# Kernel optimization log

Measured on AMD Instinct MI355X. Metric: run time of the kernel, lower is better.

## Reference

```python
import jax, jax.numpy as jnp
import numpy as np

DIM = 384; HEADS = 12; HD = DIM // HEADS; WS = 7; SHIFT = 3
RES = (14, 14, 14); N = WS ** 3; HID = 4 * DIM
NW = (RES[0] // WS) * (RES[1] // WS) * (RES[2] // WS)


def _np_attn_mask():
    Z, H, W = RES
    img = np.zeros((Z, H, W), np.float32)
    sl = (slice(0, -WS), slice(-WS, -SHIFT), slice(-SHIFT, None))
    cnt = 0
    for z in sl:
        for h in sl:
            for w in sl:
                img[z, h, w] = cnt
                cnt += 1
    m = img.reshape(Z // WS, WS, H // WS, WS, W // WS, WS)
    m = m.transpose(0, 2, 4, 1, 3, 5).reshape(NW, N)
    d = m[:, None, :] - m[:, :, None]
    return np.where(d != 0, -100.0, 0.0).astype(np.float32)  # [NW, N, N]


def _np_cpb_table_and_index():
    # continuous relative coords table, log-spaced (SwinV2), pretrained_window_size=0 -> normalize by WS-1
    r = np.arange(-(WS - 1), WS, dtype=np.float32)
    g = np.stack(np.meshgrid(r, r, r, indexing='ij'), -1)
    g = g / (WS - 1) * 8.0
    g = np.sign(g) * np.log2(np.abs(g) + 1.0) / np.log2(8.0)
    table = g.reshape(-1, 3)  # [(2W-1)^3, 3]
    c = np.stack(np.meshgrid(np.arange(WS), np.arange(WS), np.arange(WS), indexing='ij'))
    c = c.reshape(3, -1)  # [3, N]
    rel = c[:, :, None] - c[:, None, :] + (WS - 1)
    S = 2 * WS - 1
    idx = rel[0] * S * S + rel[1] * S + rel[2]  # [N, N]
    return table.astype(np.float32), idx.astype(np.int32)

_ATTN_MASK = _np_attn_mask()
_CPB_TABLE, _REL_IDX = _np_cpb_table_and_index()


def _ln(x, g, b, eps=1e-5):
    m = jnp.mean(x, -1, keepdims=True)
    v = jnp.mean(jnp.square(x - m), -1, keepdims=True)
    return (x - m) * jax.lax.rsqrt(v + eps) * g + b


def _win_part(x):  # [B,Z,H,W,C] -> [B*NW, WS,WS,WS, C]
    B, Z, H, W, C = x.shape
    x = x.reshape(B, Z // WS, WS, H // WS, WS, W // WS, WS, C)
    return x.transpose(0, 1, 3, 5, 2, 4, 6, 7).reshape(-1, WS, WS, WS, C)


def _win_rev(w, B):  # [B*NW, WS,WS,WS, C] -> [B,Z,H,W,C]
    Z, H, W = RES
    x = w.reshape(B, Z // WS, H // WS, W // WS, WS, WS, WS, -1)
    return x.transpose(0, 1, 4, 2, 5, 3, 6, 7).reshape(B, Z, H, W, -1)


def _forward(x, qkv_w, q_bias, v_bias, logit_scale, cpb_w1, cpb_b1, cpb_w2,
             proj_w, proj_b, norm1_g, norm1_b, norm2_g, norm2_b,
             fc1_w, fc1_b, fc2_w, fc2_b):
    Z, H, W = RES
    B, L, C = x.shape
    shortcut = x
    xg = x.reshape(B, Z, H, W, C)
    xg = jnp.roll(xg, (-SHIFT, -SHIFT, -SHIFT), axis=(1, 2, 3))
    xw = _win_part(xg).reshape(-1, N, C)  # [B*NW, N, C]

    qkv_b = jnp.concatenate([q_bias, jnp.zeros_like(q_bias), v_bias])
    qkv = xw @ qkv_w.T + qkv_b
    qkv = qkv.reshape(-1, N, 3, HEADS, HD).transpose(2, 0, 3, 1, 4)
    q, k, v = qkv[0], qkv[1], qkv[2]  # [B*NW, HEADS, N, HD]

    qn = q / jnp.maximum(jnp.linalg.norm(q, axis=-1, keepdims=True), 1e-12)
    kn = k / jnp.maximum(jnp.linalg.norm(k, axis=-1, keepdims=True), 1e-12)
    scale = jnp.exp(jnp.minimum(logit_scale, np.log(100.0)))  # [HEADS,1,1]
    attn = jnp.einsum('whnd,whmd->whnm', qn, kn) * scale

    # continuous relative position bias
    tbl = jax.nn.relu(jnp.asarray(_CPB_TABLE) @ cpb_w1.T + cpb_b1) @ cpb_w2.T  # [(2W-1)^3, HEADS]
    bias = 16.0 * jax.nn.sigmoid(tbl[_REL_IDX])  # [N, N, HEADS]
    attn = attn + bias.transpose(2, 0, 1)[None]

    mask = jnp.asarray(_ATTN_MASK)  # [NW, N, N]
    attn = attn.reshape(B, NW, HEADS, N, N) + mask[None, :, None]
    attn = jax.nn.softmax(attn.reshape(-1, HEADS, N, N), axis=-1)

    out = jnp.einsum('whnm,whmd->whnd', attn, v)
    out = out.transpose(0, 2, 1, 3).reshape(-1, N, C)
    out = out @ proj_w.T + proj_b

    xg = _win_rev(out.reshape(-1, WS, WS, WS, C), B)
    xg = jnp.roll(xg, (SHIFT, SHIFT, SHIFT), axis=(1, 2, 3))
    xa = xg.reshape(B, L, C)

    x1 = shortcut + _ln(xa, norm1_g, norm1_b)
    h = jax.nn.gelu(x1 @ fc1_w.T + fc1_b, approximate=False) @ fc2_w.T + fc2_b
    return x1 + _ln(h, norm2_g, norm2_b)


def setup_inputs() -> dict:
    key = jax.random.key(0)
    ks = jax.random.split(key, 8)
    B, L = 8, RES[0] * RES[1] * RES[2]
    s = 0.02
    return {
        'x': jax.random.normal(ks[0], (B, L, DIM), jnp.float32),
        'qkv_w': jax.random.normal(ks[1], (3 * DIM, DIM), jnp.float32) * s,
        'q_bias': jnp.zeros((DIM,), jnp.float32),
        'v_bias': jnp.zeros((DIM,), jnp.float32),
        'logit_scale': jnp.full((HEADS, 1, 1), np.log(10.0), jnp.float32),
        'cpb_w1': jax.random.normal(ks[2], (512, 3), jnp.float32) * s,
        'cpb_b1': jnp.zeros((512,), jnp.float32),
        'cpb_w2': jax.random.normal(ks[3], (HEADS, 512), jnp.float32) * s,
        'proj_w': jax.random.normal(ks[4], (DIM, DIM), jnp.float32) * s,
        'proj_b': jnp.zeros((DIM,), jnp.float32),
        'norm1_g': jnp.ones((DIM,), jnp.float32),
        'norm1_b': jnp.zeros((DIM,), jnp.float32),
        'norm2_g': jnp.ones((DIM,), jnp.float32),
        'norm2_b': jnp.zeros((DIM,), jnp.float32),
        'fc1_w': jax.random.normal(ks[5], (HID, DIM), jnp.float32) * s,
        'fc1_b': jnp.zeros((HID,), jnp.float32),
        'fc2_w': jax.random.normal(ks[6], (DIM, HID), jnp.float32) * s,
        'fc2_b': jnp.zeros((DIM,), jnp.float32),
    }


def reference(x, qkv_w, q_bias, v_bias, logit_scale, cpb_w1, cpb_b1, cpb_w2,
              proj_w, proj_b, norm1_g, norm1_b, norm2_g, norm2_b,
              fc1_w, fc1_b, fc2_w, fc2_b):
    return _forward(x, qkv_w, q_bias, v_bias, logit_scale, cpb_w1, cpb_b1, cpb_w2,
                    proj_w, proj_b, norm1_g, norm1_b, norm2_g, norm2_b,
                    fc1_w, fc1_b, fc2_w, fc2_b)
```

## Files before the change

### kernel.cpp

```cpp
#include <hip/hip_runtime.h>
#include <hip/hip_bf16.h>
#include <stdint.h>

namespace {

typedef __attribute__((ext_vector_type(8))) short s8v;
typedef __attribute__((ext_vector_type(4))) float f4v;
typedef __attribute__((ext_vector_type(8))) unsigned short us8;

constexpr int kN    = 343;
constexpr size_t kPlaneE = 768ull * 343 * 32;

__device__ __forceinline__ int regionOf(int c) { return c < 7 ? 0 : (c < 11 ? 1 : 2); }

__device__ __forceinline__ int winRowMap(int wtok) {
  int w = wtok / kN, nn = wtok % kN;
  int bb = w >> 3, nwi = w & 7;
  int nz = nn / 49, nh = (nn / 7) % 7, nw = nn % 7;
  int uz = (((nwi >> 2) & 1) * 7 + nz + 3) % 14;
  int uh = (((nwi >> 1) & 1) * 7 + nh + 3) % 14;
  int uw = (((nwi     ) & 1) * 7 + nw + 3) % 14;
  return bb * 2744 + uz * 196 + uh * 14 + uw;
}

__device__ __forceinline__ unsigned short f2bf(float f) {
  union { float f; unsigned u; } a; a.f = f;
  unsigned r = a.u + 0x7fffu + ((a.u >> 16) & 1u);
  return (unsigned short)(r >> 16);
}
__device__ __forceinline__ float bf2f(unsigned short u) {
  union { unsigned u; float f; } a; a.u = ((unsigned)u) << 16; return a.f;
}

__device__ __forceinline__ void gload16(const void* g, void* l) {
  __builtin_amdgcn_global_load_lds(
      (const __attribute__((address_space(1))) unsigned int*)g,
      (__attribute__((address_space(3))) unsigned int*)l, 16, 0, 0);
}

__device__ __forceinline__ float cpbFeat(int i) {
  float v = (float)(i - 6) * (8.0f / 6.0f);
  float a = log2f(fabsf(v) + 1.0f) * (1.0f / 3.0f);
  return v < 0.0f ? -a : a;
}

__global__ __launch_bounds__(256) void cvt_bf16_kernel(
    const float* __restrict__ src, unsigned short* __restrict__ dst, int n8) {
  int i = blockIdx.x * 256 + threadIdx.x;
  if (i >= n8) return;
  const float* s = src + (size_t)i * 8;
  float4 a = *(const float4*)s;
  float4 b = *(const float4*)(s + 4);
  us8 o;
  o[0]=f2bf(a.x); o[1]=f2bf(a.y); o[2]=f2bf(a.z); o[3]=f2bf(a.w);
  o[4]=f2bf(b.x); o[5]=f2bf(b.y); o[6]=f2bf(b.z); o[7]=f2bf(b.w);
  *(us8*)(dst + (size_t)i * 8) = o;
}

__global__ __launch_bounds__(256) void gather_x_kernel(
    const float* __restrict__ x, unsigned short* __restrict__ xg) {
  int chunk = blockIdx.x * 256 + threadIdx.x;
  if (chunk >= 21952 * 48) return;
  int wtok = chunk / 48, c = (chunk - wtok * 48) * 8;
  long row = winRowMap(wtok);
  const float* s = x + row * 384 + c;
  float4 a = *(const float4*)s;
  float4 b = *(const float4*)(s + 4);
  us8 o;
  o[0]=f2bf(a.x); o[1]=f2bf(a.y); o[2]=f2bf(a.z); o[3]=f2bf(a.w);
  o[4]=f2bf(b.x); o[5]=f2bf(b.y); o[6]=f2bf(b.z); o[7]=f2bf(b.w);
  *(us8*)(xg + (size_t)wtok * 384 + c) = o;
}

__global__ __launch_bounds__(256) void cpb_table_kernel(
    const float* __restrict__ w1, const float* __restrict__ b1,
    const float* __restrict__ w2, float* __restrict__ tbl) {
  int t = blockIdx.x * 256 + threadIdx.x;
  if (t >= 2197 * 12) return;
  int row = t / 12, h = t - (t / 12) * 12;
  float f0 = cpbFeat(row / 169), f1 = cpbFeat((row / 13) % 13), f2 = cpbFeat(row % 13);
  float acc = 0.f;
  for (int j = 0; j < 512; ++j) {
    float hid = fmaf(f0, w1[j*3+0], fmaf(f1, w1[j*3+1], fmaf(f2, w1[j*3+2], b1[j])));
    hid = fmaxf(hid, 0.f);
    acc = fmaf(hid, w2[h*512 + j], acc);
  }
  tbl[row * 12 + h] = acc;
}

__global__ __launch_bounds__(256) void cpb_bias_frag_kernel(
    const float* __restrict__ tbl, float* __restrict__ biasf) {
  int gid = blockIdx.x * 256 + threadIdx.x;
  if (gid >= 12 * 22 * 22 * 64) return;
  int lane = gid & 63, tile = gid >> 6;
  int jt = tile % 22, it = (tile / 22) % 22, h = tile / 484;
  int j = jt * 16 + (lane & 15);
  float v[4];
  #pragma unroll
  for (int r = 0; r < 4; ++r) {
    int i = it * 16 + (lane >> 4) * 4 + r;
    float val = -30000.f;
    if (i < kN && j < kN) {
      int iz = i/49, ih = (i/7)%7, iw = i%7;
      int jz = j/49, jh = (j/7)%7, jw = j%7;
      int idx = (iz-jz+6)*169 + (ih-jh+6)*13 + (iw-jw+6);
      float tv = tbl[idx*12 + h];
      val = 16.f / (1.f + __expf(-tv));
    }
    v[r] = val;
  }
  float4* dst = (float4*)(biasf + ((size_t)tile << 8) + (lane << 2));
  *dst = make_float4(v[0], v[1], v[2], v[3]);
}

template <int MODE>
__global__ __launch_bounds__(256) void gemm_bf16(
    const unsigned short* __restrict__ A, const unsigned short* __restrict__ W,
    const float* __restrict__ b0, const float* __restrict__ b1,
    void* __restrict__ outv, int K, int N) {
  __shared__ __align__(16) unsigned short As[2][64][32];
  __shared__ __align__(16) unsigned short Bs[2][128][32];
  const int tid = threadIdx.x, lane = tid & 63, wid = tid >> 6;
  const int wr = wid >> 1, wc = wid & 1;
  const int lr = lane & 15, lc = lane >> 4;
  const int m0 = blockIdx.y * 64, n0 = blockIdx.x * 128;

  const int sr = lane >> 2, sc = (lane & 3) << 3;
  const unsigned short* ga  = A + (size_t)(m0 + wid * 16 + sr) * K + sc;
  const unsigned short* gb0 = W + (size_t)(n0 + wid * 32 + sr) * K + sc;
  const unsigned short* gb1 = gb0 + (size_t)16 * K;

  f4v acc[2][4];
  const f4v zero4 = {0.f, 0.f, 0.f, 0.f};
  #pragma unroll
  for (int i = 0; i < 2; ++i)
    #pragma unroll
    for (int j = 0; j < 4; ++j) acc[i][j] = zero4;

  const int nk = K >> 5;
  gload16(ga,  &As[0][wid*16][0]);
  gload16(gb0, &Bs[0][wid*32][0]);
  gload16(gb1, &Bs[0][wid*32 + 16][0]);
  __syncthreads();
  for (int kt = 0; kt < nk; ++kt) {
    int cur = kt & 1;
    if (kt + 1 < nk) {
      gload16(ga  + (kt+1)*32, &As[cur^1][wid*16][0]);
      gload16(gb0 + (kt+1)*32, &Bs[cur^1][wid*32][0]);
      gload16(gb1 + (kt+1)*32, &Bs[cur^1][wid*32 + 16][0]);
    }
    s8v af0 = *(const s8v*)&As[cur][wr*32 + lr][lc*8];
    s8v af1 = *(const s8v*)&As[cur][wr*32 + 16 + lr][lc*8];
    #pragma unroll
    for (int ni = 0; ni < 4; ++ni) {
      s8v bf = *(const s8v*)&Bs[cur][wc*64 + ni*16 + lr][lc*8];
      acc[0][ni] = __builtin_amdgcn_mfma_f32_16x16x32_bf16(af0, bf, acc[0][ni], 0, 0, 0);
      acc[1][ni] = __builtin_amdgcn_mfma_f32_16x16x32_bf16(af1, bf, acc[1][ni], 0, 0, 0);
    }
    __syncthreads();
  }

  if (MODE == 0) {
    unsigned short* qkv = (unsigned short*)outv;
    #pragma unroll
    for (int mi = 0; mi < 2; ++mi)
      #pragma unroll
      for (int ni = 0; ni < 4; ++ni) {
        int cg = n0 + wc*64 + ni*16 + lr;
        int which = cg / 384, rem = cg - which * 384;
        const float* bp = (which == 0) ? b0 : (which == 2 ? b1 : nullptr);
        float badd = bp ? bp[rem] : 0.f;
        unsigned short* plane = qkv + (size_t)which * kPlaneE;
        #pragma unroll
        for (int r = 0; r < 4; ++r) {
          int mg = m0 + wr*32 + mi*16 + lc*4 + r;
          int w = mg / kN, nn = mg - w * kN;
          plane[((size_t)(w * 12 + (rem >> 5)) * kN + nn) * 32 + (rem & 31)] =
              f2bf(acc[mi][ni][r] + badd);
        }
      }
  } else {
    #pragma unroll
    for (int mi = 0; mi < 2; ++mi)
      #pragma unroll
      for (int ni = 0; ni < 4; ++ni) {
        int cg = n0 + wc*64 + ni*16 + lr;
        float badd = b0[cg];
        #pragma unroll
        for (int r = 0; r < 4; ++r) {
          size_t mg = (size_t)(m0 + wr*32 + mi*16 + lc*4 + r);
          float t = acc[mi][ni][r] + badd;
          if (MODE == 2) {
            t = 0.5f * t * (1.f + erff(t * 0.70710678118f));
            ((unsigned short*)outv)[mg * N + cg] = f2bf(t);
          } else {
            ((float*)outv)[mg * N + cg] = t;
          }
        }
      }
  }
}

__global__ __launch_bounds__(512) void attn_mfma(
    const unsigned short* __restrict__ qp, const unsigned short* __restrict__ kp,
    const unsigned short* __restrict__ vp, const float* __restrict__ biasf,
    const float* __restrict__ ls, unsigned short* __restrict__ outb) {
  __shared__ __align__(16) unsigned short Ksh[352][40];
  __shared__ __align__(16) unsigned short Vt[32][360];
  __shared__ __align__(16) unsigned short ps[8][16][360];
  __shared__ float qinvS[352], kinvS[352], cntS[352];

  const int wh = blockIdx.x;
  const int w = wh / 12, h = wh - w * 12;
  const int nwi = w & 7;
  const int tid = threadIdx.x, lane = tid & 63, wid = tid >> 6;
  const unsigned short* qb = qp + (size_t)wh * kN * 32;
  const unsigned short* kb = kp + (size_t)wh * kN * 32;
  const unsigned short* vb = vp + (size_t)wh * kN * 32;
  const float scale = __expf(fminf(ls[h], 4.6051702f));

  for (int idx = tid; idx < 1408; idx += 512) {
    int r = idx >> 2, c8 = (idx & 3) << 3;
    us8 v = {0,0,0,0,0,0,0,0};
    if (r < kN) v = *(const us8*)(kb + r * 32 + c8);
    *(us8*)&Ksh[r][c8] = v;
  }
  for (int idx = tid; idx < 32 * 17; idx += 512) {
    int d = idx / 17, c = kN + (idx - (idx / 17) * 17);
    Vt[d][c] = 0;
  }
  for (int idx = tid; idx < 1372; idx += 512) {
    int r = idx >> 2, c8 = (idx & 3) << 3;
    us8 v = *(const us8*)(vb + r * 32 + c8);
    #pragma unroll
    for (int e = 0; e < 8; ++e) Vt[c8 + e][r] = v[e];
  }
  for (int t = tid; t < 352; t += 512) {
    if (t < kN) {
      float qs = 0.f, ks = 0.f;
      #pragma unroll
      for (int c8 = 0; c8 < 4; ++c8) {
        us8 qv = *(const us8*)(qb + t * 32 + c8 * 8);
        us8 kv = *(const us8*)(kb + t * 32 + c8 * 8);
        #pragma unroll
        for (int e = 0; e < 8; ++e) {
          float f = bf2f(qv[e]); qs = fmaf(f, f, qs);
          float g = bf2f(kv[e]); ks = fmaf(g, g, ks);
        }
      }
      qinvS[t] = scale / fmaxf(sqrtf(qs), 1e-12f);
      kinvS[t] = 1.f / fmaxf(sqrtf(ks), 1e-12f);
      int jz = t / 49, jh = (t / 7) % 7, jw = t % 7;
      cntS[t] = (float)(regionOf(((nwi >> 2) & 1) * 7 + jz) * 9 +
                        regionOf(((nwi >> 1) & 1) * 7 + jh) * 3 +
                        regionOf(((nwi     ) & 1) * 7 + jw));
    } else {
      qinvS[t] = 1.f; kinvS[t] = 0.f; cntS[t] = 0.f;
    }
  }
  __syncthreads();

  const int lr = lane & 15, lc = lane >> 4;
  const f4v zero4 = {0.f, 0.f, 0.f, 0.f};

  for (int mt = wid; mt < 22; mt += 8) {
    const int i0 = mt * 16;
    s8v qa = *(const s8v*)(qb + (size_t)(i0 + lr) * 32 + lc * 8);
    float qi[4], ci[4];
    #pragma unroll
    for (int r = 0; r < 4; ++r) {
      qi[r] = qinvS[i0 + lc * 4 + r];
      ci[r] = cntS[i0 + lc * 4 + r];
    }
    float sreg[22][4];
    #pragma unroll
    for (int jt = 0; jt < 22; ++jt) {
      s8v kf = *(const s8v*)&Ksh[jt * 16 + lr][lc * 8];
      f4v s4 = __builtin_amdgcn_mfma_f32_16x16x32_bf16(qa, kf, zero4, 0, 0, 0);
      float kj = kinvS[jt * 16 + lr];
      float cj = cntS[jt * 16 + lr];
      float4 bq = *(const float4*)(biasf + (((size_t)(h * 22 + mt) * 22 + jt) << 8) + (lane << 2));
      sreg[jt][0] = s4[0] * qi[0] * kj + bq.x + ((cj != ci[0]) ? -100.f : 0.f);
      sreg[jt][1] = s4[1] * qi[1] * kj + bq.y + ((cj != ci[1]) ? -100.f : 0.f);
      sreg[jt][2] = s4[2] * qi[2] * kj + bq.z + ((cj != ci[2]) ? -100.f : 0.f);
      sreg[jt][3] = s4[3] * qi[3] * kj + bq.w + ((cj != ci[3]) ? -100.f : 0.f);
    }
    float mx[4] = {-3e38f, -3e38f, -3e38f, -3e38f};
    #pragma unroll
    for (int jt = 0; jt < 22; ++jt)
      #pragma unroll
      for (int r = 0; r < 4; ++r) mx[r] = fmaxf(mx[r], sreg[jt][r]);
    #pragma unroll
    for (int off = 1; off < 16; off <<= 1)
      #pragma unroll
      for (int r = 0; r < 4; ++r) mx[r] = fmaxf(mx[r], __shfl_xor(mx[r], off));
    float sum[4] = {0.f, 0.f, 0.f, 0.f};
    #pragma unroll
    for (int jt = 0; jt < 22; ++jt)
      #pragma unroll
      for (int r = 0; r < 4; ++r) {
        float p = __expf(sreg[jt][r] - mx[r]);
        sum[r] += p;
        ps[wid][lc * 4 + r][jt * 16 + lr] = f2bf(p);
      }
    #pragma unroll
    for (int off = 1; off < 16; off <<= 1)
      #pragma unroll
      for (int r = 0; r < 4; ++r) sum[r] += __shfl_xor(sum[r], off);
    float rinv[4];
    #pragma unroll
    for (int r = 0; r < 4; ++r) rinv[r] = 1.f / sum[r];

    f4v o0 = zero4, o1 = zero4;
    #pragma unroll
    for (int ks = 0; ks < 11; ++ks) {
      s8v pa = *(const s8v*)&ps[wid][lr][ks * 32 + lc * 8];
      s8v v0 = *(const s8v*)&Vt[lr][ks * 32 + lc * 8];
      s8v v1 = *(const s8v*)&Vt[16 + lr][ks * 32 + lc * 8];
      o0 = __builtin_amdgcn_mfma_f32_16x16x32_bf16(pa, v0, o0, 0, 0, 0);
      o1 = __builtin_amdgcn_mfma_f32_16x16x32_bf16(pa, v1, o1, 0, 0, 0);
    }
    #pragma unroll
    for (int r = 0; r < 4; ++r) {
      int i = i0 + lc * 4 + r;
      if (i < kN) {
        size_t base = ((size_t)(w * kN + i)) * 384 + h * 32;
        outb[base + lr]      = f2bf(o0[r] * rinv[r]);
        outb[base + 16 + lr] = f2bf(o1[r] * rinv[r]);
      }
    }
  }
}

template <int GATHER, int WBF>
__global__ __launch_bounds__(64) void ln_kernel(
    const float* __restrict__ src, const float* __restrict__ resid,
    const float* __restrict__ g, const float* __restrict__ b,
    float* __restrict__ out, unsigned short* __restrict__ outbf) {
  int row = blockIdx.x, lane = threadIdx.x;
  long dst = GATHER ? (long)winRowMap(row) : (long)row;
  float t[6];
  float sum = 0.f, sq = 0.f;
  #pragma unroll
  for (int i = 0; i < 6; ++i) {
    t[i] = src[(long)row * 384 + i * 64 + lane];
    sum += t[i];
    sq = fmaf(t[i], t[i], sq);
  }
  #pragma unroll
  for (int o = 32; o; o >>= 1) { sum += __shfl_xor(sum, o); sq += __shfl_xor(sq, o); }
  float mean = sum * (1.f / 384.f);
  float var = sq * (1.f / 384.f) - mean * mean;
  float rs = rsqrtf(var + 1e-5f);
  #pragma unroll
  for (int i = 0; i < 6; ++i) {
    int c = i * 64 + lane;
    float val = resid[dst * 384 + c] + (t[i] - mean) * rs * g[c] + b[c];
    out[dst * 384 + c] = val;
    if (WBF) outbf[dst * 384 + c] = f2bf(val);
  }
}

}

extern "C" void kernel_launch(void* const* d_in, const int* in_sizes, int n_in,
                              void* d_out, int out_size, void* d_ws, size_t ws_size,
                              hipStream_t stream) {
  const float* x      = (const float*)d_in[0];
  const float* qkv_w  = (const float*)d_in[1];
  const float* q_bias = (const float*)d_in[2];
  const float* v_bias = (const float*)d_in[3];
  const float* lscale = (const float*)d_in[4];
  const float* cpb_w1 = (const float*)d_in[5];
  const float* cpb_b1 = (const float*)d_in[6];
  const float* cpb_w2 = (const float*)d_in[7];
  const float* proj_w = (const float*)d_in[8];
  const float* proj_b = (const float*)d_in[9];
  const float* n1g    = (const float*)d_in[10];
  const float* n1b    = (const float*)d_in[11];
  const float* n2g    = (const float*)d_in[12];
  const float* n2b    = (const float*)d_in[13];
  const float* fc1_w  = (const float*)d_in[14];
  const float* fc1_b  = (const float*)d_in[15];
  const float* fc2_w  = (const float*)d_in[16];
  const float* fc2_b  = (const float*)d_in[17];
  float* outp = (float*)d_out;
  char* wsb = (char*)d_ws;

  float*          biasf = (float*)(wsb + 0);
  float*          tbl   = (float*)(wsb + 5947392);
  unsigned short* qkvp  = (unsigned short*)(wsb + 6052864);
  unsigned short* xg    = (unsigned short*)(wsb + 56630272);
  unsigned short* attno = (unsigned short*)(wsb + 73489408);
  unsigned short* wts   = (unsigned short*)(wsb + 90348544);
  float*          projt = (float*)(wsb + 93887488);
  float*          x1    = (float*)(wsb + 127605760);
  unsigned short* x1b   = (unsigned short*)(wsb + 161324032);
  unsigned short* hbuf  = qkvp;
  float*          h2    = projt;

  unsigned short* wq  = wts;
  unsigned short* wpj = wts + 442368;
  unsigned short* wf1 = wts + 589824;
  unsigned short* wf2 = wts + 1179648;

  cvt_bf16_kernel<<<216, 256, 0, stream>>>(qkv_w, wq, 55296);
  cvt_bf16_kernel<<<72,  256, 0, stream>>>(proj_w, wpj, 18432);
  cvt_bf16_kernel<<<288, 256, 0, stream>>>(fc1_w, wf1, 73728);
  cvt_bf16_kernel<<<288, 256, 0, stream>>>(fc2_w, wf2, 73728);
  gather_x_kernel<<<4116, 256, 0, stream>>>(x, xg);
  cpb_table_kernel<<<103, 256, 0, stream>>>(cpb_w1, cpb_b1, cpb_w2, tbl);
  cpb_bias_frag_kernel<<<1452, 256, 0, stream>>>(tbl, biasf);

  gemm_bf16<0><<<dim3(9, 343), 256, 0, stream>>>(xg, wq, q_bias, v_bias, qkvp, 384, 1152);

  attn_mfma<<<768, 512, 0, stream>>>(qkvp, qkvp + kPlaneE, qkvp + 2 * kPlaneE,
                                     biasf, lscale, attno);

  gemm_bf16<1><<<dim3(3, 343), 256, 0, stream>>>(attno, wpj, proj_b, nullptr, projt, 384, 384);

  ln_kernel<1, 1><<<21952, 64, 0, stream>>>(projt, x, n1g, n1b, x1, x1b);

  gemm_bf16<2><<<dim3(12, 343), 256, 0, stream>>>(x1b, wf1, fc1_b, nullptr, hbuf, 384, 1536);

  gemm_bf16<1><<<dim3(3, 343), 256, 0, stream>>>(hbuf, wf2, fc2_b, nullptr, h2, 1536, 384);

  ln_kernel<0, 0><<<21952, 64, 0, stream>>>(h2, x1, n2g, n2b, outp, nullptr);
}
```

Baseline: 360.8 us.

## Enlarge GEMM tiles, rework attention softmax in registers, pack LayerNorm rows

GEMM tiles grow from 64x128 to 128x128, so each block computes a 4x4 MFMA fragment grid and the grid shrinks to 172 row blocks, with padded rows guarded in the QKV epilogue. Attention now pre-normalises K in LDS and folds the Q norm, the logit scale and log2(e) into Q. It computes S transposed, so the softmax probabilities stay in registers as 16x16x16 MFMA operands instead of going through shared memory, and it uses exp2 and packed bf16 converts. LayerNorm packs 4 rows per 256-thread block, and the attention grid is reordered head-major. The padded GEMM rows read and write past the valid data, which is why the workspace offsets were enlarged.

Result: slower. 391.2 us (+8.4%).

```diff
diff --git a/kernel.cpp b/kernel.cpp
--- a/kernel.cpp
+++ b/kernel.cpp
@@ -5,11 +5,15 @@
 namespace {
 
 typedef __attribute__((ext_vector_type(8))) short s8v;
+typedef __attribute__((ext_vector_type(4))) short s4v;
 typedef __attribute__((ext_vector_type(4))) float f4v;
 typedef __attribute__((ext_vector_type(8))) unsigned short us8;
 
-constexpr int kN    = 343;
+constexpr int kN = 343;
 constexpr size_t kPlaneE = 768ull * 343 * 32;
+constexpr int kM = 21952;
+constexpr int kMp = 22016;
+constexpr float kL2E = 1.44269504f;
 
 __device__ __forceinline__ int regionOf(int c) { return c < 7 ? 0 : (c < 11 ? 1 : 2); }
 
@@ -31,6 +35,30 @@
 __device__ __forceinline__ float bf2f(unsigned short u) {
   union { unsigned u; float f; } a; a.u = ((unsigned)u) << 16; return a.f;
 }
+__device__ __forceinline__ unsigned cvtpk(float lo, float hi) {
+  unsigned r;
+  asm("v_cvt_pk_bf16_f32 %0, %1, %2" : "=v"(r) : "v"(lo), "v"(hi));
+  return r;
+}
+__device__ __forceinline__ float fexp2(float x) {
+#if __has_builtin(__builtin_amdgcn_exp2f)
+  return __builtin_amdgcn_exp2f(x);
+#else
+  return exp2f(x);
+#endif
+}
+
+#if __has_builtin(__builtin_amdgcn_mfma_f32_16x16x16bf16_1k)
+__device__ __forceinline__ f4v mfma16(s4v a, s4v b, f4v c) {
+  return __builtin_amdgcn_mfma_f32_16x16x16bf16_1k(a, b, c, 0, 0, 0);
+}
+#else
+__device__ __forceinline__ f4v mfma16(s4v a, s4v b, f4v c) {
+  f4v d;
+  asm("v_mfma_f32_16x16x16_bf16 %0, %1, %2, %3" : "=v"(d) : "v"(a), "v"(b), "v"(c));
+  return d;
+}
+#endif
 
 __device__ __forceinline__ void gload16(const void* g, void* l) {
   __builtin_amdgcn_global_load_lds(
@@ -60,7 +88,7 @@
 __global__ __launch_bounds__(256) void gather_x_kernel(
     const float* __restrict__ x, unsigned short* __restrict__ xg) {
   int chunk = blockIdx.x * 256 + threadIdx.x;
-  if (chunk >= 21952 * 48) return;
+  if (chunk >= kM * 48) return;
   int wtok = chunk / 48, c = (chunk - wtok * 48) * 8;
   long row = winRowMap(wtok);
   const float* s = x + row * 384 + c;
@@ -93,24 +121,24 @@
   int gid = blockIdx.x * 256 + threadIdx.x;
   if (gid >= 12 * 22 * 22 * 64) return;
   int lane = gid & 63, tile = gid >> 6;
-  int jt = tile % 22, it = (tile / 22) % 22, h = tile / 484;
-  int j = jt * 16 + (lane & 15);
+  int jt = tile % 22, qt = (tile / 22) % 22, h = tile / 484;
+  int i = qt * 16 + (lane & 15);
+  int j0 = jt * 16 + ((lane >> 4) << 2);
   float v[4];
   #pragma unroll
   for (int r = 0; r < 4; ++r) {
-    int i = it * 16 + (lane >> 4) * 4 + r;
-    float val = -30000.f;
+    int j = j0 + r;
+    float val = -43000.f;
     if (i < kN && j < kN) {
       int iz = i/49, ih = (i/7)%7, iw = i%7;
       int jz = j/49, jh = (j/7)%7, jw = j%7;
       int idx = (iz-jz+6)*169 + (ih-jh+6)*13 + (iw-jw+6);
       float tv = tbl[idx*12 + h];
-      val = 16.f / (1.f + __expf(-tv));
+      val = (16.f / (1.f + __expf(-tv))) * kL2E;
     }
     v[r] = val;
   }
-  float4* dst = (float4*)(biasf + ((size_t)tile << 8) + (lane << 2));
-  *dst = make_float4(v[0], v[1], v[2], v[3]);
+  *(float4*)(biasf + ((size_t)tile << 8) + (lane << 2)) = make_float4(v[0], v[1], v[2], v[3]);
 }
 
 template <int MODE>
@@ -118,78 +146,85 @@
     const unsigned short* __restrict__ A, const unsigned short* __restrict__ W,
     const float* __restrict__ b0, const float* __restrict__ b1,
     void* __restrict__ outv, int K, int N) {
-  __shared__ __align__(16) unsigned short As[2][64][32];
+  __shared__ __align__(16) unsigned short As[2][128][32];
   __shared__ __align__(16) unsigned short Bs[2][128][32];
   const int tid = threadIdx.x, lane = tid & 63, wid = tid >> 6;
   const int wr = wid >> 1, wc = wid & 1;
-  const int lr = lane & 15, lc = lane >> 4;
-  const int m0 = blockIdx.y * 64, n0 = blockIdx.x * 128;
-
-  const int sr = lane >> 2, sc = (lane & 3) << 3;
-  const unsigned short* ga  = A + (size_t)(m0 + wid * 16 + sr) * K + sc;
-  const unsigned short* gb0 = W + (size_t)(n0 + wid * 32 + sr) * K + sc;
-  const unsigned short* gb1 = gb0 + (size_t)16 * K;
-
-  f4v acc[2][4];
+  const int lq = lane & 15, gq = lane >> 4;
+  const int m0 = blockIdx.y * 128, n0 = blockIdx.x * 128;
+
+  const int r0 = tid >> 2, c0 = (tid & 3) << 3;
+  const unsigned short* gA0 = A + (size_t)(m0 + r0) * K + c0;
+  const unsigned short* gA1 = A + (size_t)(m0 + 64 + r0) * K + c0;
+  const unsigned short* gB0 = W + (size_t)(n0 + r0) * K + c0;
+  const unsigned short* gB1 = W + (size_t)(n0 + 64 + r0) * K + c0;
+
+  f4v acc[4][4];
   const f4v zero4 = {0.f, 0.f, 0.f, 0.f};
   #pragma unroll
-  for (int i = 0; i < 2; ++i)
+  for (int i = 0; i < 4; ++i)
     #pragma unroll
     for (int j = 0; j < 4; ++j) acc[i][j] = zero4;
 
   const int nk = K >> 5;
-  gload16(ga,  &As[0][wid*16][0]);
-  gload16(gb0, &Bs[0][wid*32][0]);
-  gload16(gb1, &Bs[0][wid*32 + 16][0]);
+#define STAGE(buf, kt)                                         \
+  gload16(gA0 + (kt) * 32, &As[buf][r0][c0]);                  \
+  gload16(gA1 + (kt) * 32, &As[buf][64 + r0][c0]);             \
+  gload16(gB0 + (kt) * 32, &Bs[buf][r0][c0]);                  \
+  gload16(gB1 + (kt) * 32, &Bs[buf][64 + r0][c0]);
+
+  STAGE(0, 0);
   __syncthreads();
   for (int kt = 0; kt < nk; ++kt) {
     int cur = kt & 1;
-    if (kt + 1 < nk) {
-      gload16(ga  + (kt+1)*32, &As[cur^1][wid*16][0]);
-      gload16(gb0 + (kt+1)*32, &Bs[cur^1][wid*32][0]);
-      gload16(gb1 + (kt+1)*32, &Bs[cur^1][wid*32 + 16][0]);
-    }
-    s8v af0 = *(const s8v*)&As[cur][wr*32 + lr][lc*8];
-    s8v af1 = *(const s8v*)&As[cur][wr*32 + 16 + lr][lc*8];
-    #pragma unroll
-    for (int ni = 0; ni < 4; ++ni) {
-      s8v bf = *(const s8v*)&Bs[cur][wc*64 + ni*16 + lr][lc*8];
-      acc[0][ni] = __builtin_amdgcn_mfma_f32_16x16x32_bf16(af0, bf, acc[0][ni], 0, 0, 0);
-      acc[1][ni] = __builtin_amdgcn_mfma_f32_16x16x32_bf16(af1, bf, acc[1][ni], 0, 0, 0);
+    if (kt + 1 < nk) { STAGE(cur ^ 1, kt + 1); }
+    s8v af[4];
+    #pragma unroll
+    for (int mt = 0; mt < 4; ++mt)
+      af[mt] = *(const s8v*)&As[cur][wr * 64 + mt * 16 + lq][gq * 8];
+    #pragma unroll
+    for (int nt = 0; nt < 4; ++nt) {
+      s8v bfr = *(const s8v*)&Bs[cur][wc * 64 + nt * 16 + lq][gq * 8];
+      #pragma unroll
+      for (int mt = 0; mt < 4; ++mt)
+        acc[mt][nt] = __builtin_amdgcn_mfma_f32_16x16x32_bf16(af[mt], bfr, acc[mt][nt], 0, 0, 0);
     }
     __syncthreads();
   }
+#undef STAGE
 
   if (MODE == 0) {
     unsigned short* qkv = (unsigned short*)outv;
     #pragma unroll
-    for (int mi = 0; mi < 2; ++mi)
-      #pragma unroll
-      for (int ni = 0; ni < 4; ++ni) {
-        int cg = n0 + wc*64 + ni*16 + lr;
-        int which = cg / 384, rem = cg - which * 384;
-        const float* bp = (which == 0) ? b0 : (which == 2 ? b1 : nullptr);
-        float badd = bp ? bp[rem] : 0.f;
-        unsigned short* plane = qkv + (size_t)which * kPlaneE;
+    for (int nt = 0; nt < 4; ++nt) {
+      int cg = n0 + wc * 64 + nt * 16 + lq;
+      int which = cg / 384, rem = cg - which * 384;
+      const float* bp = (which == 0) ? b0 : (which == 2 ? b1 : nullptr);
+      float badd = bp ? bp[rem] : 0.f;
+      unsigned short* plane = qkv + (size_t)which * kPlaneE;
+      #pragma unroll
+      for (int mt = 0; mt < 4; ++mt)
         #pragma unroll
         for (int r = 0; r < 4; ++r) {
-          int mg = m0 + wr*32 + mi*16 + lc*4 + r;
-          int w = mg / kN, nn = mg - w * kN;
-          plane[((size_t)(w * 12 + (rem >> 5)) * kN + nn) * 32 + (rem & 31)] =
-              f2bf(acc[mi][ni][r] + badd);
+          int mg = m0 + wr * 64 + mt * 16 + gq * 4 + r;
+          if (mg < kM) {
+            int w = mg / kN, nn = mg - w * kN;
+            plane[((size_t)(w * 12 + (rem >> 5)) * kN + nn) * 32 + (rem & 31)] =
+                f2bf(acc[mt][nt][r] + badd);
+          }
         }
-      }
+    }
   } else {
     #pragma unroll
-    for (int mi = 0; mi < 2; ++mi)
-      #pragma unroll
-      for (int ni = 0; ni < 4; ++ni) {
-        int cg = n0 + wc*64 + ni*16 + lr;
-        float badd = b0[cg];
+    for (int nt = 0; nt < 4; ++nt) {
+      int cg = n0 + wc * 64 + nt * 16 + lq;
+      float badd = b0[cg];
+      #pragma unroll
+      for (int mt = 0; mt < 4; ++mt)
         #pragma unroll
         for (int r = 0; r < 4; ++r) {
-          size_t mg = (size_t)(m0 + wr*32 + mi*16 + lc*4 + r);
-          float t = acc[mi][ni][r] + badd;
+          size_t mg = (size_t)(m0 + wr * 64 + mt * 16 + gq * 4 + r);
+          float t = acc[mt][nt][r] + badd;
           if (MODE == 2) {
             t = 0.5f * t * (1.f + erff(t * 0.70710678118f));
             ((unsigned short*)outv)[mg * N + cg] = f2bf(t);
@@ -197,7 +232,7 @@
             ((float*)outv)[mg * N + cg] = t;
           }
         }
-      }
+    }
   }
 }
 
@@ -206,138 +241,150 @@
     const unsigned short* __restrict__ vp, const float* __restrict__ biasf,
     const float* __restrict__ ls, unsigned short* __restrict__ outb) {
   __shared__ __align__(16) unsigned short Ksh[352][40];
-  __shared__ __align__(16) unsigned short Vt[32][360];
-  __shared__ __align__(16) unsigned short ps[8][16][360];
-  __shared__ float qinvS[352], kinvS[352], cntS[352];
-
-  const int wh = blockIdx.x;
-  const int w = wh / 12, h = wh - w * 12;
+  __shared__ __align__(16) unsigned short Vt[32][364];
+  __shared__ float qmulS[352];
+  __shared__ float cntS[352];
+
+  const int bid = blockIdx.x;
+  const int h = bid >> 6, w = bid & 63;
+  const int wh = w * 12 + h;
   const int nwi = w & 7;
   const int tid = threadIdx.x, lane = tid & 63, wid = tid >> 6;
+  const int lq = lane & 15, gq = lane >> 4;
   const unsigned short* qb = qp + (size_t)wh * kN * 32;
   const unsigned short* kb = kp + (size_t)wh * kN * 32;
   const unsigned short* vb = vp + (size_t)wh * kN * 32;
-  const float scale = __expf(fminf(ls[h], 4.6051702f));
+  const float sl2e = __expf(fminf(ls[h], 4.6051702f)) * kL2E;
 
   for (int idx = tid; idx < 1408; idx += 512) {
     int r = idx >> 2, c8 = (idx & 3) << 3;
-    us8 v = {0,0,0,0,0,0,0,0};
+    us8 v = {0, 0, 0, 0, 0, 0, 0, 0};
     if (r < kN) v = *(const us8*)(kb + r * 32 + c8);
     *(us8*)&Ksh[r][c8] = v;
   }
-  for (int idx = tid; idx < 32 * 17; idx += 512) {
-    int d = idx / 17, c = kN + (idx - (idx / 17) * 17);
-    Vt[d][c] = 0;
-  }
+  for (int idx = tid; idx < 288; idx += 512)
+    Vt[idx / 9][343 + (idx % 9)] = 0;
   for (int idx = tid; idx < 1372; idx += 512) {
     int r = idx >> 2, c8 = (idx & 3) << 3;
     us8 v = *(const us8*)(vb + r * 32 + c8);
     #pragma unroll
     for (int e = 0; e < 8; ++e) Vt[c8 + e][r] = v[e];
   }
-  for (int t = tid; t < 352; t += 512) {
+  __syncthreads();
+  if (tid < 352) {
+    int t = tid;
     if (t < kN) {
-      float qs = 0.f, ks = 0.f;
+      float ks = 0.f;
+      us8 kv[4];
       #pragma unroll
       for (int c8 = 0; c8 < 4; ++c8) {
-        us8 qv = *(const us8*)(qb + t * 32 + c8 * 8);
-        us8 kv = *(const us8*)(kb + t * 32 + c8 * 8);
+        kv[c8] = *(const us8*)&Ksh[t][c8 * 8];
         #pragma unroll
-        for (int e = 0; e < 8; ++e) {
-          float f = bf2f(qv[e]); qs = fmaf(f, f, qs);
-          float g = bf2f(kv[e]); ks = fmaf(g, g, ks);
-        }
+        for (int e = 0; e < 8; ++e) { float f = bf2f(kv[c8][e]); ks = fmaf(f, f, ks); }
       }
-      qinvS[t] = scale / fmaxf(sqrtf(qs), 1e-12f);
-      kinvS[t] = 1.f / fmaxf(sqrtf(ks), 1e-12f);
+      float kmul = rsqrtf(fmaxf(ks, 1e-24f));
+      #pragma unroll
+      for (int c8 = 0; c8 < 4; ++c8) {
+        us8 o;
+        #pragma unroll
+        for (int e = 0; e < 8; ++e) o[e] = f2bf(bf2f(kv[c8][e]) * kmul);
+        *(us8*)&Ksh[t][c8 * 8] = o;
+      }
+      float qs = 0.f;
+      #pragma unroll
+      for (int c8 = 0; c8 < 4; ++c8) {
+        us8 qv = *(const us8*)(qb + (size_t)t * 32 + c8 * 8);
+        #pragma unroll
+        for (int e = 0; e < 8; ++e) { float f = bf2f(qv[e]); qs = fmaf(f, f, qs); }
+      }
+      qmulS[t] = rsqrtf(fmaxf(qs, 1e-24f)) * sl2e;
       int jz = t / 49, jh = (t / 7) % 7, jw = t % 7;
       cntS[t] = (float)(regionOf(((nwi >> 2) & 1) * 7 + jz) * 9 +
                         regionOf(((nwi >> 1) & 1) * 7 + jh) * 3 +
                         regionOf(((nwi     ) & 1) * 7 + jw));
     } else {
-      qinvS[t] = 1.f; kinvS[t] = 0.f; cntS[t] = 0.f;
+      qmulS[t] = 0.f; cntS[t] = 0.f;
     }
   }
   __syncthreads();
 
-  const int lr = lane & 15, lc = lane >> 4;
   const f4v zero4 = {0.f, 0.f, 0.f, 0.f};
 
-  for (int mt = wid; mt < 22; mt += 8) {
-    const int i0 = mt * 16;
-    s8v qa = *(const s8v*)(qb + (size_t)(i0 + lr) * 32 + lc * 8);
-    float qi[4], ci[4];
+  for (int qt = wid; qt < 22; qt += 8) {
+    const int i0 = qt * 16;
+    us8 qv = *(const us8*)(qb + (size_t)(i0 + lq) * 32 + gq * 8);
+    float qm = qmulS[i0 + lq];
+    union { unsigned u[4]; s8v s; } qq;
+    #pragma unroll
+    for (int e = 0; e < 4; ++e)
+      qq.u[e] = cvtpk(bf2f(qv[2 * e]) * qm, bf2f(qv[2 * e + 1]) * qm);
+    s8v qa = qq.s;
+    float ci = cntS[i0 + lq];
+    const float* bb = biasf + (((size_t)(h * 22 + qt) * 22) << 8) + (lane << 2);
+
+    float l2[22][4];
+    #pragma unroll
+    for (int jt = 0; jt < 22; ++jt) {
+      s8v kf = *(const s8v*)&Ksh[jt * 16 + lq][gq * 8];
+      f4v s4 = __builtin_amdgcn_mfma_f32_16x16x32_bf16(kf, qa, zero4, 0, 0, 0);
+      float bqa[4];
+      *(float4*)bqa = *(const float4*)(bb + ((size_t)jt << 8));
+      #pragma unroll
+      for (int r = 0; r < 4; ++r) {
+        float cj = cntS[jt * 16 + 4 * gq + r];
+        l2[jt][r] = s4[r] + bqa[r] + ((cj != ci) ? -144.269504f : 0.f);
+      }
+    }
+    float m = -3e38f;
+    #pragma unroll
+    for (int jt = 0; jt < 22; ++jt)
+      m = fmaxf(m, fmaxf(fmaxf(l2[jt][0], l2[jt][1]), fmaxf(l2[jt][2], l2[jt][3])));
+    m = fmaxf(m, __shfl_xor(m, 16));
+    m = fmaxf(m, __shfl_xor(m, 32));
+    float sum = 0.f;
+    s4v pa[22];
+    #pragma unroll
+    for (int jt = 0; jt < 22; ++jt) {
+      float p0 = fexp2(l2[jt][0] - m), p1 = fexp2(l2[jt][1] - m);
+      float p2 = fexp2(l2[jt][2] - m), p3 = fexp2(l2[jt][3] - m);
+      sum += (p0 + p1) + (p2 + p3);
+      union { unsigned u[2]; s4v s; } pk;
+      pk.u[0] = cvtpk(p0, p1);
+      pk.u[1] = cvtpk(p2, p3);
+      pa[jt] = pk.s;
+    }
+    sum += __shfl_xor(sum, 16);
+    sum += __shfl_xor(sum, 32);
+    float rinv = 1.f / sum;
+
+    f4v o0 = zero4, o1 = zero4;
+    #pragma unroll
+    for (int jt = 0; jt < 22; ++jt) {
+      s4v v0 = *(const s4v*)&Vt[lq][jt * 16 + 4 * gq];
+      s4v v1 = *(const s4v*)&Vt[16 + lq][jt * 16 + 4 * gq];
+      o0 = mfma16(pa[jt], v0, o0);
+      o1 = mfma16(pa[jt], v1, o1);
+    }
+    asm volatile("s_nop 7\ns_nop 7" :::);
     #pragma unroll
     for (int r = 0; r < 4; ++r) {
-      qi[r] = qinvS[i0 + lc * 4 + r];
-      ci[r] = cntS[i0 + lc * 4 + r];
-    }
-    float sreg[22][4];
-    #pragma unroll
-    for (int jt = 0; jt < 22; ++jt) {
-      s8v kf = *(const s8v*)&Ksh[jt * 16 + lr][lc * 8];
-      f4v s4 = __builtin_amdgcn_mfma_f32_16x16x32_bf16(qa, kf, zero4, 0, 0, 0);
-      float kj = kinvS[jt * 16 + lr];
-      float cj = cntS[jt * 16 + lr];
-      float4 bq = *(const float4*)(biasf + (((size_t)(h * 22 + mt) * 22 + jt) << 8) + (lane << 2));
-      sreg[jt][0] = s4[0] * qi[0] * kj + bq.x + ((cj != ci[0]) ? -100.f : 0.f);
-      sreg[jt][1] = s4[1] * qi[1] * kj + bq.y + ((cj != ci[1]) ? -100.f : 0.f);
-      sreg[jt][2] = s4[2] * qi[2] * kj + bq.z + ((cj != ci[2]) ? -100.f : 0.f);
-      sreg[jt][3] = s4[3] * qi[3] * kj + bq.w + ((cj != ci[3]) ? -100.f : 0.f);
-    }
-    float mx[4] = {-3e38f, -3e38f, -3e38f, -3e38f};
-    #pragma unroll
-    for (int jt = 0; jt < 22; ++jt)
-      #pragma unroll
-      for (int r = 0; r < 4; ++r) mx[r] = fmaxf(mx[r], sreg[jt][r]);
-    #pragma unroll
-    for (int off = 1; off < 16; off <<= 1)
-      #pragma unroll
-      for (int r = 0; r < 4; ++r) mx[r] = fmaxf(mx[r], __shfl_xor(mx[r], off));
-    float sum[4] = {0.f, 0.f, 0.f, 0.f};
-    #pragma unroll
-    for (int jt = 0; jt < 22; ++jt)
-      #pragma unroll
-      for (int r = 0; r < 4; ++r) {
-        float p = __expf(sreg[jt][r] - mx[r]);
-        sum[r] += p;
-        ps[wid][lc * 4 + r][jt * 16 + lr] = f2bf(p);
+      int q = i0 + 4 * gq + r;
+      float rv = __shfl(rinv, 4 * gq + r);
+      if (q < kN) {
+        size_t base = ((size_t)(w * kN + q)) * 384 + h * 32;
+        outb[base + lq]      = f2bf(o0[r] * rv);
+        outb[base + 16 + lq] = f2bf(o1[r] * rv);
       }
-    #pragma unroll
-    for (int off = 1; off < 16; off <<= 1)
-      #pragma unroll
-      for (int r = 0; r < 4; ++r) sum[r] += __shfl_xor(sum[r], off);
-    float rinv[4];
-    #pragma unroll
-    for (int r = 0; r < 4; ++r) rinv[r] = 1.f / sum[r];
-
-    f4v o0 = zero4, o1 = zero4;
-    #pragma unroll
-    for (int ks = 0; ks < 11; ++ks) {
-      s8v pa = *(const s8v*)&ps[wid][lr][ks * 32 + lc * 8];
-      s8v v0 = *(const s8v*)&Vt[lr][ks * 32 + lc * 8];
-      s8v v1 = *(const s8v*)&Vt[16 + lr][ks * 32 + lc * 8];
-      o0 = __builtin_amdgcn_mfma_f32_16x16x32_bf16(pa, v0, o0, 0, 0, 0);
-      o1 = __builtin_amdgcn_mfma_f32_16x16x32_bf16(pa, v1, o1, 0, 0, 0);
-    }
-    #pragma unroll
-    for (int r = 0; r < 4; ++r) {
-      int i = i0 + lc * 4 + r;
-      if (i < kN) {
-        size_t base = ((size_t)(w * kN + i)) * 384 + h * 32;
-        outb[base + lr]      = f2bf(o0[r] * rinv[r]);
-        outb[base + 16 + lr] = f2bf(o1[r] * rinv[r]);
-      }
     }
   }
 }
 
 template <int GATHER, int WBF>
-__global__ __launch_bounds__(64) void ln_kernel(
+__global__ __launch_bounds__(256) void ln_kernel(
     const float* __restrict__ src, const float* __restrict__ resid,
     const float* __restrict__ g, const float* __restrict__ b,
     float* __restrict__ out, unsigned short* __restrict__ outbf) {
-  int row = blockIdx.x, lane = threadIdx.x;
+  int row = blockIdx.x * 4 + (threadIdx.x >> 6), lane = threadIdx.x & 63;
   long dst = GATHER ? (long)winRowMap(row) : (long)row;
   float t[6];
   float sum = 0.f, sq = 0.f;
@@ -391,11 +438,11 @@
   float*          tbl   = (float*)(wsb + 5947392);
   unsigned short* qkvp  = (unsigned short*)(wsb + 6052864);
   unsigned short* xg    = (unsigned short*)(wsb + 56630272);
-  unsigned short* attno = (unsigned short*)(wsb + 73489408);
-  unsigned short* wts   = (unsigned short*)(wsb + 90348544);
-  float*          projt = (float*)(wsb + 93887488);
-  float*          x1    = (float*)(wsb + 127605760);
-  unsigned short* x1b   = (unsigned short*)(wsb + 161324032);
+  unsigned short* attno = (unsigned short*)(wsb + 73538560);
+  unsigned short* wts   = (unsigned short*)(wsb + 90446848);
+  float*          projt = (float*)(wsb + 93985792);
+  float*          x1    = (float*)(wsb + 127802368);
+  unsigned short* x1b   = (unsigned short*)(wsb + 161520640);
   unsigned short* hbuf  = qkvp;
   float*          h2    = projt;
 
@@ -412,18 +459,18 @@
   cpb_table_kernel<<<103, 256, 0, stream>>>(cpb_w1, cpb_b1, cpb_w2, tbl);
   cpb_bias_frag_kernel<<<1452, 256, 0, stream>>>(tbl, biasf);
 
-  gemm_bf16<0><<<dim3(9, 343), 256, 0, stream>>>(xg, wq, q_bias, v_bias, qkvp, 384, 1152);
+  gemm_bf16<0><<<dim3(9, 172), 256, 0, stream>>>(xg, wq, q_bias, v_bias, qkvp, 384, 1152);
 
   attn_mfma<<<768, 512, 0, stream>>>(qkvp, qkvp + kPlaneE, qkvp + 2 * kPlaneE,
                                      biasf, lscale, attno);
 
-  gemm_bf16<1><<<dim3(3, 343), 256, 0, stream>>>(attno, wpj, proj_b, nullptr, projt, 384, 384);
-
-  ln_kernel<1, 1><<<21952, 64, 0, stream>>>(projt, x, n1g, n1b, x1, x1b);
-
-  gemm_bf16<2><<<dim3(12, 343), 256, 0, stream>>>(x1b, wf1, fc1_b, nullptr, hbuf, 384, 1536);
-
-  gemm_bf16<1><<<dim3(3, 343), 256, 0, stream>>>(hbuf, wf2, fc2_b, nullptr, h2, 1536, 384);
-
-  ln_kernel<0, 0><<<21952, 64, 0, stream>>>(h2, x1, n2g, n2b, outp, nullptr);
-}
+  gemm_bf16<1><<<dim3(3, 172), 256, 0, stream>>>(attno, wpj, proj_b, nullptr, projt, 384, 384);
+
+  ln_kernel<1, 1><<<5488, 256, 0, stream>>>(projt, x, n1g, n1b, x1, x1b);
+
+  gemm_bf16<2><<<dim3(12, 172), 256, 0, stream>>>(x1b, wf1, fc1_b, nullptr, hbuf, 384, 1536);
+
+  gemm_bf16<1><<<dim3(3, 172), 256, 0, stream>>>(hbuf, wf2, fc2_b, nullptr, h2, 1536, 384);
+
+  ln_kernel<0, 0><<<5488, 256, 0, stream>>>(h2, x1, n2g, n2b, outp, nullptr);
+}
```
